# Performance work log

Hardware: AMD Instinct MI355X
Metric: run time of the kernel (lower is better)

The kernel has to match this reference:

```python
import jax, jax.numpy as jnp
import numpy as np

EPS = 1e-7
ALPHA = 16.0
RANK = 64
CURV = 1.0


def lorentz_expmap0(x, c):
    # x: [N, d] tangent at origin (spatial part). Returns [N, d+1] point on hyperboloid.
    sc = jnp.sqrt(c)
    vn = jnp.maximum(jnp.linalg.norm(x, axis=-1, keepdims=True), EPS)  # [N,1]
    t = jnp.cosh(sc * vn) / sc                                        # [N,1] time coord
    sp = (jnp.sinh(sc * vn) / (sc * vn)) * x                          # [N,d] spatial
    return jnp.concatenate([t, sp], axis=-1)


def lorentz_recompute_time(s, c):
    # s: [N, d] spatial part. time = sqrt(1/c + ||s||^2) so <p,p>_L = -1/c.
    sq = jnp.sum(s * s, axis=-1, keepdims=True)
    t = jnp.sqrt(1.0 / c + sq)
    return jnp.concatenate([t, s], axis=-1)


def lorentz_logmap0(p, c):
    # p: [N, d+1] on hyperboloid. Returns [N, d] tangent (spatial) at origin.
    sc = jnp.sqrt(c)
    t = p[:, :1]
    y = p[:, 1:]
    yn = jnp.maximum(jnp.linalg.norm(y, axis=-1, keepdims=True), EPS)
    arg = jnp.maximum(sc * t, 1.0 + EPS)  # arccosh domain clamp
    d = jnp.arccosh(arg) / sc             # geodesic distance from origin
    return (d / yn) * y


def setup_inputs() -> dict:
    key = jax.random.key(0)
    k1, k2, k3 = jax.random.split(key, 3)
    N, D_IN, D_OUT, R = 16384, 4096, 4096, RANK
    x = jax.random.normal(k1, (N, D_IN), dtype=jnp.float32) * 0.02
    # torch Linear weight layout: A_w [r, in], B_w [out, r]
    A_w = jax.random.normal(k2, (R, D_IN), dtype=jnp.float32) * (1.0 / np.sqrt(D_IN))
    B_w = jax.random.normal(k3, (D_OUT, R), dtype=jnp.float32) * (1.0 / np.sqrt(R))
    return {"x": x, "A_w": A_w, "B_w": B_w}


def reference(x, A_w, B_w):
    c = CURV
    p0 = lorentz_expmap0(x, c)                    # [N, D_IN+1]
    s1 = p0[:, 1:] @ A_w.T                        # [N, R]
    p1 = lorentz_recompute_time(s1, c)            # [N, R+1]
    s2 = p1[:, 1:] @ B_w.T                        # [N, D_OUT]
    p2 = lorentz_recompute_time(s2, c)            # [N, D_OUT+1]
    v = lorentz_logmap0(p2, c)                    # [N, D_OUT]
    return (ALPHA / RANK) * v
```

## Files before the change

### kernel.cpp

```cpp
#include <hip/hip_runtime.h>
#include <hip/hip_bf16.h>

#define NROWS 16384
#define DIN   4096
#define DOUT  4096
#define RNK   64
#define EPSF  1e-7f

typedef float  f32x4  __attribute__((ext_vector_type(4)));
typedef __bf16 bf16x4 __attribute__((ext_vector_type(4)));
typedef __bf16 bf16x8 __attribute__((ext_vector_type(8)));

__device__ __forceinline__ bf16x8 cvt8(f32x4 a, f32x4 b) {
    bf16x8 r;
    r[0]=(__bf16)a.x; r[1]=(__bf16)a.y; r[2]=(__bf16)a.z; r[3]=(__bf16)a.w;
    r[4]=(__bf16)b.x; r[5]=(__bf16)b.y; r[6]=(__bf16)b.z; r[7]=(__bf16)b.w;
    return r;
}

__global__ __launch_bounds__(512, 4)
void kb_gram(const float* __restrict__ Bw, __bf16* __restrict__ Bpf,
             float* __restrict__ Gpart) {
    __shared__ __bf16 bs[256][72];
    const int t = threadIdx.x;
    const int jb = blockIdx.x * 256;

    {
        const int j0 = t >> 1, c0 = (t & 1) * 32;
        #pragma unroll
        for (int u = 0; u < 4; ++u) {
            f32x4 v0 = *(const f32x4*)&Bw[(size_t)(jb + j0) * RNK + c0 + 8*u];
            f32x4 v1 = *(const f32x4*)&Bw[(size_t)(jb + j0) * RNK + c0 + 8*u + 4];
            *(bf16x8*)&bs[j0][c0 + 8*u] = cvt8(v0, v1);
        }
    }
    __syncthreads();

    #pragma unroll
    for (int u = 0; u < 4; ++u) {
        const int lc = t + 512 * u;
        const int ll = lc & 63;
        const int ks = (lc >> 6) & 1;
        const int jl = lc >> 7;
        bf16x8 v = *(const bf16x8*)&bs[jl * 16 + (ll & 15)][ks * 32 + (ll >> 4) * 8];
        const size_t C = ((size_t)((jb >> 4) + jl) * 2 + ks) * 64 + ll;
        *(bf16x8*)&Bpf[C * 8] = v;
    }

    const int r = t & 63, rp = (t >> 6) * 8;
    float acc[8] = {0,0,0,0,0,0,0,0};
    for (int j = 0; j < 256; ++j) {
        float s = (float)bs[j][r];
        bf16x8 v = *(const bf16x8*)&bs[j][rp];
        #pragma unroll
        for (int u = 0; u < 8; ++u) acc[u] += s * (float)v[u];
    }
    #pragma unroll
    for (int u = 0; u < 8; ++u)
        Gpart[(size_t)blockIdx.x * 4096 + r * 64 + rp + u] = acc[u];
}

__global__ void kc0_sum(const float* __restrict__ Gpart, float* __restrict__ G) {
    const int t = threadIdx.x;
    #pragma unroll
    for (int v = 0; v < 4; ++v) {
        f32x4 a = {0.f, 0.f, 0.f, 0.f};
        for (int b = 0; b < 16; ++b)
            a += *(const f32x4*)&Gpart[(size_t)b * 4096 + t * 16 + v * 4];
        *(f32x4*)&G[t * 16 + v * 4] = a;
    }
}

#define LPK 136
__global__ __launch_bounds__(512, 4)
void kfused(const float* __restrict__ x, const float* __restrict__ Aw,
            const float* __restrict__ G, const __bf16* __restrict__ Bpf,
            float* __restrict__ out) {
    __shared__ __align__(16) char smem[28928];
    __bf16 (*xs)[LPK]      = (__bf16 (*)[LPK])(smem);
    __bf16 (*as)[LPK]      = (__bf16 (*)[LPK])(smem + 8704);
    float  (*Gs)[64]       = (float (*)[64])(smem);
    float  (*s1f)[64]      = (float (*)[64])(smem + 16384);
    __bf16 (*s1pf)[2][64][8] = (__bf16 (*)[2][64][8])(smem + 24576);
    float  *rowss          = (float*)(smem + 28672);
    float  *gsc            = (float*)(smem + 28800);

    const int t = threadIdx.x;
    const int l = t & 63;
    const int w = t >> 6;
    const int brow = blockIdx.x * 32;

    const int xrow = t >> 4, xcol = (t & 15) * 8;
    const int arow = t >> 3, acol = (t & 7) * 16;
    const size_t xb = (size_t)(brow + xrow) * DIN + xcol;
    const size_t ab = (size_t)arow * DIN + acol;

    const int m0   = (w & 1) * 16;
    const int n0   = (w >> 1) * 16;
    const int frow = l & 15;
    const int koff = (l >> 4) * 8;

    float ssq = 0.f;
    f32x4 acc = {0.f, 0.f, 0.f, 0.f};
    f32x4 xA0,xA1,aA0,aA1,aA2,aA3, xB0,xB1,aB0,aB1,aB2,aB3;

    auto load = [&](f32x4&x0,f32x4&x1,f32x4&A0,f32x4&A1,f32x4&A2,f32x4&A3,int kt){
        const size_t o = (size_t)kt * 128;
        x0 = *(const f32x4*)&x[xb + o];       x1 = *(const f32x4*)&x[xb + o + 4];
        A0 = *(const f32x4*)&Aw[ab + o];      A1 = *(const f32x4*)&Aw[ab + o + 4];
        A2 = *(const f32x4*)&Aw[ab + o + 8];  A3 = *(const f32x4*)&Aw[ab + o + 12];
    };
    auto consume = [&](const f32x4&x0,const f32x4&x1,const f32x4&A0,
                       const f32x4&A1,const f32x4&A2,const f32x4&A3){
        ssq += x0.x*x0.x + x0.y*x0.y + x0.z*x0.z + x0.w*x0.w;
        ssq += x1.x*x1.x + x1.y*x1.y + x1.z*x1.z + x1.w*x1.w;
        *(bf16x8*)&xs[xrow][xcol]     = cvt8(x0, x1);
        *(bf16x8*)&as[arow][acol]     = cvt8(A0, A1);
        *(bf16x8*)&as[arow][acol + 8] = cvt8(A2, A3);
        __syncthreads();
        #pragma unroll
        for (int ks = 0; ks < 4; ++ks) {
            bf16x8 af  = *(const bf16x8*)&xs[m0 + frow][ks*32 + koff];
            bf16x8 bf_ = *(const bf16x8*)&as[n0 + frow][ks*32 + koff];
            acc = __builtin_amdgcn_mfma_f32_16x16x32_bf16(af, bf_, acc, 0, 0, 0);
        }
        __syncthreads();
    };

    const int NT = DIN / 128;
    load(xA0,xA1,aA0,aA1,aA2,aA3, 0);
    for (int kt = 0; kt < NT; kt += 2) {
        load(xB0,xB1,aB0,aB1,aB2,aB3, kt + 1);
        consume(xA0,xA1,aA0,aA1,aA2,aA3);
        if (kt + 2 < NT) load(xA0,xA1,aA0,aA1,aA2,aA3, kt + 2);
        consume(xB0,xB1,aB0,aB1,aB2,aB3);
    }

    {
        float* gf = &Gs[0][0];
        *(f32x4*)&gf[t * 8]     = *(const f32x4*)&G[t * 8];
        *(f32x4*)&gf[t * 8 + 4] = *(const f32x4*)&G[t * 8 + 4];
    }
    ssq += __shfl_xor(ssq, 1);
    ssq += __shfl_xor(ssq, 2);
    ssq += __shfl_xor(ssq, 4);
    ssq += __shfl_xor(ssq, 8);
    if ((l & 15) == 0) rowss[w * 4 + (l >> 4)] = ssq;
    __syncthreads();
    if (t < 32) {
        float vn = fmaxf(sqrtf(rowss[t]), EPSF);
        rowss[t] = sinhf(vn) / vn;
    }
    __syncthreads();

    #pragma unroll
    for (int q = 0; q < 4; ++q) {
        const int row = m0 + (l >> 4) * 4 + q;
        s1f[row][n0 + frow] = rowss[row] * acc[q];
    }
    __syncthreads();

    {
        const int r0 = w * 4;
        float y0=0.f, y1=0.f, y2=0.f, y3=0.f;
        for (int r = 0; r < 64; ++r) {
            const float gr = Gs[r][l];
            y0 += gr * s1f[r0 + 0][r];
            y1 += gr * s1f[r0 + 1][r];
            y2 += gr * s1f[r0 + 2][r];
            y3 += gr * s1f[r0 + 3][r];
        }
        float q0 = s1f[r0 + 0][l] * y0;
        float q1 = s1f[r0 + 1][l] * y1;
        float q2 = s1f[r0 + 2][l] * y2;
        float q3 = s1f[r0 + 3][l] * y3;
        #pragma unroll
        for (int s = 1; s < 64; s <<= 1) {
            q0 += __shfl_xor(q0, s);
            q1 += __shfl_xor(q1, s);
            q2 += __shfl_xor(q2, s);
            q3 += __shfl_xor(q3, s);
        }
        if (l == 0) {
            float r2v[4] = {q0, q1, q2, q3};
            #pragma unroll
            for (int i = 0; i < 4; ++i) {
                const float r2 = r2v[i];
                const float rn = sqrtf(r2);
                gsc[r0 + i] = 0.25f * acoshf(fmaxf(sqrtf(1.f + r2), 1.f + EPSF))
                                    / fmaxf(rn, EPSF);
            }
        }
    }
    __syncthreads();

    if (t < 256) {
        const int ll = t & 63, ksq = (t >> 6) & 1, mg = t >> 7;
        const int row = mg * 16 + (ll & 15);
        const int kc  = ksq * 32 + (ll >> 4) * 8;
        const float gg = gsc[row];
        bf16x8 p;
        #pragma unroll
        for (int u = 0; u < 8; ++u) p[u] = (__bf16)(gg * s1f[row][kc + u]);
        *(bf16x8*)&s1pf[mg][ksq][ll][0] = p;
    }
    __syncthreads();

    {
        const int mg = w & 1;
        const int mr0 = mg * 16;
        const bf16x8 a0f = *(const bf16x8*)&s1pf[mg][0][l][0];
        const bf16x8 a1f = *(const bf16x8*)&s1pf[mg][1][l][0];
        #pragma unroll 4
        for (int jj = 0; jj < 64; ++jj) {
            const int j = (w >> 1) + jj * 4;
            const size_t base = ((size_t)j * 2 * 64 + l) * 8;
            bf16x8 b0 = *(const bf16x8*)&Bpf[base];
            bf16x8 b1 = *(const bf16x8*)&Bpf[base + 512];
            f32x4 a2 = {0.f, 0.f, 0.f, 0.f};
            a2 = __builtin_amdgcn_mfma_f32_16x16x32_bf16(a0f, b0, a2, 0, 0, 0);
            a2 = __builtin_amdgcn_mfma_f32_16x16x32_bf16(a1f, b1, a2, 0, 0, 0);
            const int col = j * 16 + frow;
            #pragma unroll
            for (int q = 0; q < 4; ++q) {
                const int row = mr0 + (l >> 4) * 4 + q;
                out[(size_t)(brow + row) * DOUT + col] = a2[q];
            }
        }
    }
}

extern "C" void kernel_launch(void* const* d_in, const int* in_sizes, int n_in,
                              void* d_out, int out_size, void* d_ws, size_t ws_size,
                              hipStream_t stream) {
    const float* x  = (const float*)d_in[0];
    const float* Aw = (const float*)d_in[1];
    const float* Bw = (const float*)d_in[2];
    float* out = (float*)d_out;

    char* ws = (char*)d_ws;
    __bf16* Bpf   = (__bf16*)(ws);
    float*  Gpart = (float*)(ws + 524288);
    float*  G     = (float*)(ws + 786432);

    kb_gram<<<16, 512, 0, stream>>>(Bw, Bpf, Gpart);
    kc0_sum<<<1, 256, 0, stream>>>(Gpart, G);
    kfused<<<NROWS / 32, 512, 0, stream>>>(x, Aw, G, Bpf, out);
}
```

Before: 193.4 us.

## Double-buffer LDS tiles and deepen register prefetch in first GEMM loop

The x·A_w^T K-loop now alternates between two LDS buffers, so each k-step needs one barrier instead of two. A third register set holds an extra prefetched tile, and a raw s_waitcnt plus s_barrier with sched_barrier fences replaces __syncthreads. The goal is to cut barrier stalls and hide more global-load latency. In exchange, LDS per block roughly doubles and register use rises, which may lower occupancy below the launch-bounds target.

Result: no change. 194.9 us (+0.8%).

```diff
diff --git a/kernel.cpp b/kernel.cpp
--- a/kernel.cpp
+++ b/kernel.cpp
@@ -72,13 +72,12 @@
 }
 
 #define LPK 136
+#define BUFSZ 26112
 __global__ __launch_bounds__(512, 4)
 void kfused(const float* __restrict__ x, const float* __restrict__ Aw,
             const float* __restrict__ G, const __bf16* __restrict__ Bpf,
             float* __restrict__ out) {
-    __shared__ __align__(16) char smem[28928];
-    __bf16 (*xs)[LPK]      = (__bf16 (*)[LPK])(smem);
-    __bf16 (*as)[LPK]      = (__bf16 (*)[LPK])(smem + 8704);
+    __shared__ __align__(16) char smem[2 * BUFSZ];
     float  (*Gs)[64]       = (float (*)[64])(smem);
     float  (*s1f)[64]      = (float (*)[64])(smem + 16384);
     __bf16 (*s1pf)[2][64][8] = (__bf16 (*)[2][64][8])(smem + 24576);
@@ -102,7 +101,9 @@
 
     float ssq = 0.f;
     f32x4 acc = {0.f, 0.f, 0.f, 0.f};
-    f32x4 xA0,xA1,aA0,aA1,aA2,aA3, xB0,xB1,aB0,aB1,aB2,aB3;
+    f32x4 xA0,xA1,aA0,aA1,aA2,aA3;
+    f32x4 xB0,xB1,aB0,aB1,aB2,aB3;
+    f32x4 xC0,xC1,aC0,aC1,aC2,aC3;
 
     auto load = [&](f32x4&x0,f32x4&x1,f32x4&A0,f32x4&A1,f32x4&A2,f32x4&A3,int kt){
         const size_t o = (size_t)kt * 128;
@@ -111,30 +112,39 @@
         A2 = *(const f32x4*)&Aw[ab + o + 8];  A3 = *(const f32x4*)&Aw[ab + o + 12];
     };
     auto consume = [&](const f32x4&x0,const f32x4&x1,const f32x4&A0,
-                       const f32x4&A1,const f32x4&A2,const f32x4&A3){
+                       const f32x4&A1,const f32x4&A2,const f32x4&A3, int par){
+        __bf16 (*xsp)[LPK] = (__bf16 (*)[LPK])(smem + par * BUFSZ);
+        __bf16 (*asp)[LPK] = (__bf16 (*)[LPK])(smem + par * BUFSZ + 8704);
         ssq += x0.x*x0.x + x0.y*x0.y + x0.z*x0.z + x0.w*x0.w;
         ssq += x1.x*x1.x + x1.y*x1.y + x1.z*x1.z + x1.w*x1.w;
-        *(bf16x8*)&xs[xrow][xcol]     = cvt8(x0, x1);
-        *(bf16x8*)&as[arow][acol]     = cvt8(A0, A1);
-        *(bf16x8*)&as[arow][acol + 8] = cvt8(A2, A3);
-        __syncthreads();
+        *(bf16x8*)&xsp[xrow][xcol]     = cvt8(x0, x1);
+        *(bf16x8*)&asp[arow][acol]     = cvt8(A0, A1);
+        *(bf16x8*)&asp[arow][acol + 8] = cvt8(A2, A3);
+        __builtin_amdgcn_sched_barrier(0);
+        asm volatile("s_waitcnt lgkmcnt(0)" ::: "memory");
+        __builtin_amdgcn_s_barrier();
+        __builtin_amdgcn_sched_barrier(0);
         #pragma unroll
         for (int ks = 0; ks < 4; ++ks) {
-            bf16x8 af  = *(const bf16x8*)&xs[m0 + frow][ks*32 + koff];
-            bf16x8 bf_ = *(const bf16x8*)&as[n0 + frow][ks*32 + koff];
+            bf16x8 af  = *(const bf16x8*)&xsp[m0 + frow][ks*32 + koff];
+            bf16x8 bf_ = *(const bf16x8*)&asp[n0 + frow][ks*32 + koff];
             acc = __builtin_amdgcn_mfma_f32_16x16x32_bf16(af, bf_, acc, 0, 0, 0);
         }
-        __syncthreads();
     };
 
-    const int NT = DIN / 128;
     load(xA0,xA1,aA0,aA1,aA2,aA3, 0);
-    for (int kt = 0; kt < NT; kt += 2) {
-        load(xB0,xB1,aB0,aB1,aB2,aB3, kt + 1);
-        consume(xA0,xA1,aA0,aA1,aA2,aA3);
-        if (kt + 2 < NT) load(xA0,xA1,aA0,aA1,aA2,aA3, kt + 2);
-        consume(xB0,xB1,aB0,aB1,aB2,aB3);
-    }
+    load(xB0,xB1,aB0,aB1,aB2,aB3, 1);
+    for (int kt = 0; kt < 30; kt += 3) {
+        load(xC0,xC1,aC0,aC1,aC2,aC3, kt + 2);
+        consume(xA0,xA1,aA0,aA1,aA2,aA3, kt & 1);
+        load(xA0,xA1,aA0,aA1,aA2,aA3, kt + 3);
+        consume(xB0,xB1,aB0,aB1,aB2,aB3, (kt + 1) & 1);
+        load(xB0,xB1,aB0,aB1,aB2,aB3, kt + 4);
+        consume(xC0,xC1,aC0,aC1,aC2,aC3, kt & 1);
+    }
+    consume(xA0,xA1,aA0,aA1,aA2,aA3, 0);
+    consume(xB0,xB1,aB0,aB1,aB2,aB3, 1);
+    __syncthreads();
 
     {
         float* gf = &Gs[0][0];
```
